# Performance work log

Hardware: AMD Instinct MI355X
Metric: run time of the kernel (lower is better)

## Reference

```python
import jax, jax.numpy as jnp
import numpy as np

N_NODES = 100000
N_EDGES = 1600000
D_IN = 128
D_HID = 128
D_EMB = 128
D_OUT = 16


def _glorot(key, shape):
    fan_in, fan_out = shape
    lim = (6.0 / (fan_in + fan_out)) ** 0.5
    return jax.random.uniform(key, shape, jnp.float32, -lim, lim)


def setup_inputs() -> dict:
    key = jax.random.key(0)
    ks = jax.random.split(key, 12)
    x = jax.random.normal(ks[0], (N_NODES, D_IN), jnp.float32)
    edge_index = jax.random.randint(ks[1], (2, N_EDGES), 0, N_NODES, jnp.int32)
    return {
        "x": x,
        "edge_index": edge_index,
        # SAGEConv layer 0: neighbor weight, self(root) weight, bias
        "Wn0": _glorot(ks[2], (D_IN, D_HID)),
        "Ws0": _glorot(ks[3], (D_IN, D_HID)),
        "b0": jnp.zeros((D_HID,), jnp.float32),
        # SAGEConv layer 1
        "Wn1": _glorot(ks[4], (D_HID, D_HID)),
        "Ws1": _glorot(ks[5], (D_HID, D_HID)),
        "b1": jnp.zeros((D_HID,), jnp.float32),
        # SAGEConv layer 2 (to embedding dim)
        "Wn2": _glorot(ks[6], (D_HID, D_EMB)),
        "Ws2": _glorot(ks[7], (D_HID, D_EMB)),
        "b2": jnp.zeros((D_EMB,), jnp.float32),
        # final fc
        "Wfc": _glorot(ks[8], (D_EMB, D_OUT)),
        "bfc": jnp.zeros((D_OUT,), jnp.float32),
    }


def _sage_conv(x, src, dst, deg_inv, Wn, Ws, b):
    # mean-aggregate source features at destination nodes, then transform.
    agg = jax.ops.segment_sum(x[src], dst, num_segments=N_NODES)  # [N, d]
    mean = agg * deg_inv[:, None]
    return mean @ Wn + x @ Ws + b


def reference(x, edge_index, Wn0, Ws0, b0, Wn1, Ws1, b1, Wn2, Ws2, b2, Wfc, bfc):
    src, dst = edge_index[0], edge_index[1]
    deg = jax.ops.segment_sum(jnp.ones((src.shape[0],), x.dtype), dst,
                              num_segments=N_NODES)
    deg_inv = 1.0 / jnp.maximum(deg, 1.0)

    h = _sage_conv(x, src, dst, deg_inv, Wn0, Ws0, b0)
    h = jax.nn.relu(h)  # dropout omitted (eval mode / deterministic reference)
    h = _sage_conv(h, src, dst, deg_inv, Wn1, Ws1, b1)
    h = jax.nn.relu(h)
    emb = _sage_conv(h, src, dst, deg_inv, Wn2, Ws2, b2)
    y = emb @ Wfc + bfc
    return emb, jax.nn.log_softmax(y, axis=1)
```

## Files before the change

kernel.cpp:

```cpp
#include <hip/hip_runtime.h>
#include <hip/hip_fp16.h>

#define NN 100000
#define NE 1600000
#define DD 128
#define CAP 64
#define FRAG_ELEMS 16384

#define NRNG 8
#define RNODES 12500
#define EPT 8
#define FILL_T (NE / EPT)
#define FILL_BPR ((FILL_T + 255) / 256)

typedef __attribute__((ext_vector_type(8))) _Float16 half8;
typedef __attribute__((ext_vector_type(4))) float f32x4;

__global__ void k_xcast(const float* __restrict__ x, _Float16* __restrict__ xh,
                        int* __restrict__ cnt) {
    int t = blockIdx.x * 256 + threadIdx.x;
    if (t < NN) cnt[t] = 0;
    const float* p = x + (size_t)t * 8;
    float4 v0 = *(const float4*)p;
    float4 v1 = *(const float4*)(p + 4);
    half8 o = { (_Float16)v0.x, (_Float16)v0.y, (_Float16)v0.z, (_Float16)v0.w,
                (_Float16)v1.x, (_Float16)v1.y, (_Float16)v1.z, (_Float16)v1.w };
    *(half8*)(xh + (size_t)t * 8) = o;
}

__global__ __launch_bounds__(256) void k_fill(const int* __restrict__ src,
                                              const int* __restrict__ dst,
                                              int* __restrict__ cnt,
                                              int* __restrict__ bkt) {
    int rng = blockIdx.x & (NRNG - 1);
    int t = (blockIdx.x >> 3) * 256 + threadIdx.x;
    if (t >= FILL_T) return;
    int lo = rng * RNODES;
    const int4* d4 = (const int4*)dst;
    const int4* s4 = (const int4*)src;
    int4 d0 = d4[t * 2];
    int4 d1 = d4[t * 2 + 1];
    int4 s0 = s4[t * 2];
    int4 s1 = s4[t * 2 + 1];
    int dd[8] = { d0.x, d0.y, d0.z, d0.w, d1.x, d1.y, d1.z, d1.w };
    int ss[8] = { s0.x, s0.y, s0.z, s0.w, s1.x, s1.y, s1.z, s1.w };
#pragma unroll
    for (int k = 0; k < 8; ++k) {
        int d = dd[k];
        unsigned rel = (unsigned)(d - lo);
        if (rel < (unsigned)RNODES) {
            int p = atomicAdd(&cnt[d], 1);
            if (p < CAP) bkt[(size_t)d * CAP + p] = ss[k];
        }
    }
}

__global__ __launch_bounds__(256) void k_wprep(const float* __restrict__ W0,
                                               const float* __restrict__ W1,
                                               const float* __restrict__ W2,
                                               const float* __restrict__ W3,
                                               const float* __restrict__ W4,
                                               const float* __restrict__ W5,
                                               _Float16* __restrict__ out) {
    int mat = blockIdx.x >> 6;
    int e = (blockIdx.x & 63) * 256 + threadIdx.x;
    const float* W = (mat == 0) ? W0 : (mat == 1) ? W1 : (mat == 2) ? W2
                   : (mat == 3) ? W3 : (mat == 4) ? W4 : W5;
    int j = e & 7;
    int lane = (e >> 3) & 63;
    int ct = (e >> 9) & 7;
    int kt = e >> 12;
    int k = kt * 32 + (lane >> 4) * 8 + j;
    int n = ct * 16 + (lane & 15);
    float v = W[k * 128 + n];
    _Float16 hi = (_Float16)v;
    _Float16 lo = (_Float16)(v - (float)hi);
    _Float16* mb = out + (size_t)mat * 2 * FRAG_ELEMS;
    mb[e] = hi;
    mb[FRAG_ELEMS + e] = lo;
}

__global__ __launch_bounds__(256) void k_agg(const _Float16* __restrict__ h,
                                             const int* __restrict__ cnt,
                                             const int* __restrict__ bkt,
                                             _Float16* __restrict__ mean) {
    int node = blockIdx.x * 4 + (threadIdx.x >> 6);
    if (node >= NN) return;
    int lane = threadIdx.x & 63;
    int q = lane >> 4;
    int col = (lane & 15) * 8;
    int deg = cnt[node];
    int n = deg > CAP ? CAP : deg;
    const int* b = bkt + (size_t)node * CAP;
    float a[8] = {};
    int i = 0;
    for (; i + 8 <= n; i += 8) {
        int s0 = b[i + q];
        int s1 = b[i + 4 + q];
        half8 v0 = *(const half8*)(h + (size_t)s0 * DD + col);
        half8 v1 = *(const half8*)(h + (size_t)s1 * DD + col);
#pragma unroll
        for (int j = 0; j < 8; ++j) a[j] += (float)v0[j] + (float)v1[j];
    }
    if (i + 4 <= n) {
        int s0 = b[i + q];
        half8 v0 = *(const half8*)(h + (size_t)s0 * DD + col);
#pragma unroll
        for (int j = 0; j < 8; ++j) a[j] += (float)v0[j];
        i += 4;
    }
    if (i + q < n) {
        int s = b[i + q];
        half8 v = *(const half8*)(h + (size_t)s * DD + col);
#pragma unroll
        for (int j = 0; j < 8; ++j) a[j] += (float)v[j];
    }
#pragma unroll
    for (int j = 0; j < 8; ++j) {
        a[j] += __shfl_xor(a[j], 16);
        a[j] += __shfl_xor(a[j], 32);
    }
    if (q == 0) {
        float di = 1.0f / (float)(deg > 1 ? deg : 1);
        half8 o;
#pragma unroll
        for (int j = 0; j < 8; ++j) o[j] = (_Float16)(a[j] * di);
        *(half8*)(mean + (size_t)node * DD + col) = o;
    }
}

__global__ __launch_bounds__(256) void k_gemm(
    const _Float16* __restrict__ meanp, const _Float16* __restrict__ hin,
    const _Float16* __restrict__ wf,
    const float* __restrict__ bias,
    _Float16* __restrict__ outh, float* __restrict__ outf) {

    __shared__ _Float16 sw[2][4096];

    int t = threadIdx.x;
    int wave = t >> 6;
    int lane = t & 63;
    int m16 = lane & 15;
    int kg = lane >> 4;
    int rowA = blockIdx.x * 64 + wave * 16 + m16;
    if (rowA >= NN) rowA = NN - 1;

    f32x4 acc[8] = {};

    for (int s = 0; s < 2; ++s) {
        const _Float16* Whi = wf + s * 2 * FRAG_ELEMS;
        const _Float16* Wlo = Whi + FRAG_ELEMS;
        const _Float16* Ap = (s ? hin : meanp) + (size_t)rowA * DD;
#pragma unroll
        for (int kt = 0; kt < 4; ++kt) {
            __syncthreads();
            {
                const half8* srch = (const half8*)(Whi + kt * 4096);
                const half8* srcl = (const half8*)(Wlo + kt * 4096);
                half8* dsth = (half8*)sw[0];
                half8* dstl = (half8*)sw[1];
                dsth[t]       = srch[t];
                dsth[t + 256] = srch[t + 256];
                dstl[t]       = srcl[t];
                dstl[t + 256] = srcl[t + 256];
            }
            __syncthreads();
            half8 a = *(const half8*)(Ap + kt * 32 + kg * 8);
#pragma unroll
            for (int ct = 0; ct < 8; ++ct) {
                half8 bh = *(const half8*)(sw[0] + (ct * 64 + lane) * 8);
                half8 bl = *(const half8*)(sw[1] + (ct * 64 + lane) * 8);
                acc[ct] = __builtin_amdgcn_mfma_f32_16x16x32_f16(a, bh, acc[ct], 0, 0, 0);
                acc[ct] = __builtin_amdgcn_mfma_f32_16x16x32_f16(a, bl, acc[ct], 0, 0, 0);
            }
        }
    }

    int rbase = blockIdx.x * 64 + wave * 16 + kg * 4;
    if (outh) {
#pragma unroll
        for (int ct = 0; ct < 8; ++ct) {
            int col = ct * 16 + m16;
            float bv = bias[col];
#pragma unroll
            for (int i = 0; i < 4; ++i) {
                int r = rbase + i;
                if (r < NN)
                    outh[(size_t)r * DD + col] = (_Float16)fmaxf(acc[ct][i] + bv, 0.0f);
            }
        }
    } else {
#pragma unroll
        for (int ct = 0; ct < 8; ++ct) {
            int col = ct * 16 + m16;
            float bv = bias[col];
#pragma unroll
            for (int i = 0; i < 4; ++i) {
                int r = rbase + i;
                if (r < NN)
                    outf[(size_t)r * DD + col] = acc[ct][i] + bv;
            }
        }
    }
}

__global__ __launch_bounds__(256) void k_fc(const float* __restrict__ emb,
                                            const float* __restrict__ Wfc,
                                            const float* __restrict__ bfc,
                                            float* __restrict__ out) {
    __shared__ float se[16 * 128];
    __shared__ float swt[128 * 16];
    int t = threadIdx.x;
    int nb = blockIdx.x * 16;
    int idx = t * 8;
    *(float4*)(se + idx)      = *(const float4*)(emb + (size_t)nb * 128 + idx);
    *(float4*)(se + idx + 4)  = *(const float4*)(emb + (size_t)nb * 128 + idx + 4);
    *(float4*)(swt + idx)     = *(const float4*)(Wfc + idx);
    *(float4*)(swt + idx + 4) = *(const float4*)(Wfc + idx + 4);
    __syncthreads();

    int nl = t >> 4;
    int o = t & 15;
    float acc = bfc[o];
    const float* er = se + nl * 128;
#pragma unroll 8
    for (int k = 0; k < 128; ++k)
        acc += er[k] * swt[k * 16 + o];

    float m = acc;
#pragma unroll
    for (int d = 1; d < 16; d <<= 1) m = fmaxf(m, __shfl_xor(m, d, 16));
    float e = expf(acc - m);
    float ssum = e;
#pragma unroll
    for (int d = 1; d < 16; d <<= 1) ssum += __shfl_xor(ssum, d, 16);
    out[(size_t)(nb + nl) * 16 + o] = (acc - m) - logf(ssum);
}

extern "C" void kernel_launch(void* const* d_in, const int* in_sizes, int n_in,
                              void* d_out, int out_size, void* d_ws, size_t ws_size,
                              hipStream_t stream) {
    const float* x   = (const float*)d_in[0];
    const int*   ei  = (const int*)d_in[1];
    const float* Wn0 = (const float*)d_in[2];
    const float* Ws0 = (const float*)d_in[3];
    const float* b0  = (const float*)d_in[4];
    const float* Wn1 = (const float*)d_in[5];
    const float* Ws1 = (const float*)d_in[6];
    const float* b1  = (const float*)d_in[7];
    const float* Wn2 = (const float*)d_in[8];
    const float* Ws2 = (const float*)d_in[9];
    const float* b2  = (const float*)d_in[10];
    const float* Wfc = (const float*)d_in[11];
    const float* bfc = (const float*)d_in[12];

    const int* src = ei;
    const int* dst = ei + NE;

    float* emb_out = (float*)d_out;
    float* lsm_out = emb_out + (size_t)NN * 128;

    char* ws = (char*)d_ws;
    _Float16* xh    = (_Float16*)(ws);
    _Float16* hA    = (_Float16*)(ws + 25600000);
    _Float16* hB    = (_Float16*)(ws + 51200000);
    _Float16* mean  = (_Float16*)(ws + 76800000);
    int*      cnt   = (int*)     (ws + 102400000);
    int*      bkt   = (int*)     (ws + 102800000);
    _Float16* wfrag = (_Float16*)(ws + 128400000);

    k_xcast<<<(NN * DD / 8) / 256, 256, 0, stream>>>(x, xh, cnt);
    k_wprep<<<384, 256, 0, stream>>>(Wn0, Ws0, Wn1, Ws1, Wn2, Ws2, wfrag);
    k_fill<<<NRNG * FILL_BPR, 256, 0, stream>>>(src, dst, cnt, bkt);

    const int agg_blocks  = (NN + 3) / 4;
    const int gemm_blocks = (NN + 63) / 64;
    _Float16* wf0 = wfrag;
    _Float16* wf1 = wfrag + 4 * FRAG_ELEMS;
    _Float16* wf2 = wfrag + 8 * FRAG_ELEMS;

    k_agg<<<agg_blocks, 256, 0, stream>>>(xh, cnt, bkt, mean);
    k_gemm<<<gemm_blocks, 256, 0, stream>>>(mean, xh, wf0, b0, hA, nullptr);

    k_agg<<<agg_blocks, 256, 0, stream>>>(hA, cnt, bkt, mean);
    k_gemm<<<gemm_blocks, 256, 0, stream>>>(mean, hA, wf1, b1, hB, nullptr);

    k_agg<<<agg_blocks, 256, 0, stream>>>(hB, cnt, bkt, mean);
    k_gemm<<<gemm_blocks, 256, 0, stream>>>(mean, hB, wf2, b2, nullptr, emb_out);

    k_fc<<<NN / 16, 256, 0, stream>>>(emb_out, Wfc, bfc, lsm_out);
}
```

Before: 495.5 us.

## Store hidden features in 16-column slices to shrink gather working set

```diff
diff --git a/kernel.cpp b/kernel.cpp
--- a/kernel.cpp
+++ b/kernel.cpp
@@ -13,19 +13,26 @@
 #define FILL_T (NE / EPT)
 #define FILL_BPR ((FILL_T + 255) / 256)
 
+#define SLICE_STRIDE ((size_t)NN * 16)
+
 typedef __attribute__((ext_vector_type(8))) _Float16 half8;
+typedef __attribute__((ext_vector_type(4))) _Float16 half4;
 typedef __attribute__((ext_vector_type(4))) float f32x4;
 
 __global__ void k_xcast(const float* __restrict__ x, _Float16* __restrict__ xh,
                         int* __restrict__ cnt) {
     int t = blockIdx.x * 256 + threadIdx.x;
     if (t < NN) cnt[t] = 0;
-    const float* p = x + (size_t)t * 8;
+    int node = t >> 4;
+    int cg = t & 15;
+    int s = cg >> 1;
+    int off = (cg & 1) * 8;
+    const float* p = x + (size_t)node * 128 + cg * 8;
     float4 v0 = *(const float4*)p;
     float4 v1 = *(const float4*)(p + 4);
     half8 o = { (_Float16)v0.x, (_Float16)v0.y, (_Float16)v0.z, (_Float16)v0.w,
                 (_Float16)v1.x, (_Float16)v1.y, (_Float16)v1.z, (_Float16)v1.w };
-    *(half8*)(xh + (size_t)t * 8) = o;
+    *(half8*)(xh + (size_t)s * SLICE_STRIDE + (size_t)node * 16 + off) = o;
 }
 
 __global__ __launch_bounds__(256) void k_fill(const int* __restrict__ src,
@@ -84,48 +91,39 @@
                                              const int* __restrict__ cnt,
                                              const int* __restrict__ bkt,
                                              _Float16* __restrict__ mean) {
-    int node = blockIdx.x * 4 + (threadIdx.x >> 6);
+    int s = blockIdx.x & 7;
+    int node = (blockIdx.x >> 3) * 4 + (threadIdx.x >> 6);
     if (node >= NN) return;
     int lane = threadIdx.x & 63;
-    int q = lane >> 4;
-    int col = (lane & 15) * 8;
+    int g = lane >> 2;
+    int c = lane & 3;
+    const _Float16* hs = h + (size_t)s * SLICE_STRIDE;
     int deg = cnt[node];
     int n = deg > CAP ? CAP : deg;
     const int* b = bkt + (size_t)node * CAP;
-    float a[8] = {};
-    int i = 0;
-    for (; i + 8 <= n; i += 8) {
-        int s0 = b[i + q];
-        int s1 = b[i + 4 + q];
-        half8 v0 = *(const half8*)(h + (size_t)s0 * DD + col);
-        half8 v1 = *(const half8*)(h + (size_t)s1 * DD + col);
-#pragma unroll
-        for (int j = 0; j < 8; ++j) a[j] += (float)v0[j] + (float)v1[j];
-    }
-    if (i + 4 <= n) {
-        int s0 = b[i + q];
-        half8 v0 = *(const half8*)(h + (size_t)s0 * DD + col);
-#pragma unroll
-        for (int j = 0; j < 8; ++j) a[j] += (float)v0[j];
-        i += 4;
-    }
-    if (i + q < n) {
-        int s = b[i + q];
-        half8 v = *(const half8*)(h + (size_t)s * DD + col);
-#pragma unroll
-        for (int j = 0; j < 8; ++j) a[j] += (float)v[j];
-    }
-#pragma unroll
-    for (int j = 0; j < 8; ++j) {
+    float a[4] = {};
+    for (int i = 0; i < n; i += 16) {
+        int e = i + g;
+        if (e < n) {
+            int src = __builtin_nontemporal_load(&b[e]);
+            half4 v = *(const half4*)(hs + (size_t)src * 16 + c * 4);
+#pragma unroll
+            for (int j = 0; j < 4; ++j) a[j] += (float)v[j];
+        }
+    }
+#pragma unroll
+    for (int j = 0; j < 4; ++j) {
+        a[j] += __shfl_xor(a[j], 4);
+        a[j] += __shfl_xor(a[j], 8);
         a[j] += __shfl_xor(a[j], 16);
         a[j] += __shfl_xor(a[j], 32);
     }
-    if (q == 0) {
+    if (g == 0) {
         float di = 1.0f / (float)(deg > 1 ? deg : 1);
-        half8 o;
-#pragma unroll
-        for (int j = 0; j < 8; ++j) o[j] = (_Float16)(a[j] * di);
-        *(half8*)(mean + (size_t)node * DD + col) = o;
+        half4 o = { (_Float16)(a[0] * di), (_Float16)(a[1] * di),
+                    (_Float16)(a[2] * di), (_Float16)(a[3] * di) };
+        __builtin_nontemporal_store(o,
+            (half4*)(mean + (size_t)s * SLICE_STRIDE + (size_t)node * 16 + c * 4));
     }
 }
 
@@ -145,12 +143,16 @@
     int rowA = blockIdx.x * 64 + wave * 16 + m16;
     if (rowA >= NN) rowA = NN - 1;
 
+    int shalf = kg >> 1;
+    int aoff = (kg & 1) * 8;
+    size_t rowterm = (size_t)rowA * 16 + aoff;
+
     f32x4 acc[8] = {};
 
     for (int s = 0; s < 2; ++s) {
         const _Float16* Whi = wf + s * 2 * FRAG_ELEMS;
         const _Float16* Wlo = Whi + FRAG_ELEMS;
-        const _Float16* Ap = (s ? hin : meanp) + (size_t)rowA * DD;
+        const _Float16* Ap = (s ? hin : meanp);
 #pragma unroll
         for (int kt = 0; kt < 4; ++kt) {
             __syncthreads();
@@ -165,7 +167,7 @@
                 dstl[t + 256] = srcl[t + 256];
             }
             __syncthreads();
-            half8 a = *(const half8*)(Ap + kt * 32 + kg * 8);
+            half8 a = *(const half8*)(Ap + (size_t)(kt * 2 + shalf) * SLICE_STRIDE + rowterm);
 #pragma unroll
             for (int ct = 0; ct < 8; ++ct) {
                 half8 bh = *(const half8*)(sw[0] + (ct * 64 + lane) * 8);
@@ -180,13 +182,13 @@
     if (outh) {
 #pragma unroll
         for (int ct = 0; ct < 8; ++ct) {
-            int col = ct * 16 + m16;
-            float bv = bias[col];
+            float bv = bias[ct * 16 + m16];
+            _Float16* os = outh + (size_t)ct * SLICE_STRIDE;
 #pragma unroll
             for (int i = 0; i < 4; ++i) {
                 int r = rbase + i;
                 if (r < NN)
-                    outh[(size_t)r * DD + col] = (_Float16)fmaxf(acc[ct][i] + bv, 0.0f);
+                    os[(size_t)r * 16 + m16] = (_Float16)fmaxf(acc[ct][i] + bv, 0.0f);
             }
         }
     } else {
@@ -269,11 +271,11 @@
     int*      bkt   = (int*)     (ws + 102800000);
     _Float16* wfrag = (_Float16*)(ws + 128400000);
 
-    k_xcast<<<(NN * DD / 8) / 256, 256, 0, stream>>>(x, xh, cnt);
+    k_xcast<<<(NN * 16) / 256, 256, 0, stream>>>(x, xh, cnt);
     k_wprep<<<384, 256, 0, stream>>>(Wn0, Ws0, Wn1, Ws1, Wn2, Ws2, wfrag);
     k_fill<<<NRNG * FILL_BPR, 256, 0, stream>>>(src, dst, cnt, bkt);
 
-    const int agg_blocks  = (NN + 3) / 4;
+    const int agg_blocks  = ((NN + 3) / 4) * 8;
     const int gemm_blocks = (NN + 63) / 64;
     _Float16* wf0 = wfrag;
     _Float16* wf1 = wfrag + 4 * FRAG_ELEMS;
```

Measured after the change: 1.046 ms. 111% more time.
